# Kernel optimization log

Hardware: AMD Instinct MI355X
Metric: run time of the kernel (lower is better)

The kernel has to match this reference:

```python
import jax, jax.numpy as jnp
import numpy as np

IN_F = 8192
OUT_F = 8192
MAX_STATES = 100
THRESHOLD = MAX_STATES // 2  # 50
TARGET_FIRING_RATE = 0.1


def setup_inputs() -> dict:
    key = jax.random.key(0)
    k0, k1 = jax.random.split(key)
    spike_input = jax.random.uniform(k0, (IN_F,), dtype=jnp.float32)
    # buffer init: randint(threshold-5, threshold+5) -> values in [45, 55)
    synapse_states = jax.random.randint(k1, (OUT_F, IN_F), THRESHOLD - 5, THRESHOLD + 5).astype(jnp.float32)
    membrane_potential = jnp.zeros((OUT_F,), dtype=jnp.float32)
    adaptive_threshold = jnp.full((OUT_F,), 2.0, dtype=jnp.float32)
    eligibility_trace = jnp.zeros((OUT_F, IN_F), dtype=jnp.float32)
    return {
        "spike_input": spike_input,
        "synapse_states": synapse_states,
        "membrane_potential": membrane_potential,
        "adaptive_threshold": adaptive_threshold,
        "eligibility_trace": eligibility_trace,
    }


def reference(spike_input, synapse_states, membrane_potential, adaptive_threshold, eligibility_trace):
    # ternary (0/1) weights from state threshold
    w = (synapse_states > THRESHOLD).astype(jnp.float32)  # [out, in]
    x = jnp.clip(spike_input * 2.0, 0.0, 1.0)             # [in]
    current = jnp.einsum('oi,i->o', w, x)                 # [out]
    v_mem = membrane_potential * 0.7 + current            # decayed membrane + input current
    spikes = (v_mem >= adaptive_threshold).astype(jnp.float32)
    new_threshold = jnp.clip(adaptive_threshold + (spikes - TARGET_FIRING_RATE) * 0.05, 0.5, 5.0)
    new_trace = jnp.clip(eligibility_trace * 0.8 + jnp.outer(spikes, x), 0.0, 3.0)
    new_v_mem = v_mem * (1.0 - spikes) * 0.3              # reset fired neurons, leak rest
    return spikes, new_v_mem, new_threshold, new_trace
```

## Files before the change

kernel.cpp:

```cpp
#include <hip/hip_runtime.h>

#define IN_F 8192
#define OUT_F 8192
#define THRESHOLD_F 50.0f
#define TARGET_RATE 0.1f

__global__ __launch_bounds__(256, 4) void snn_fused_kernel(
    const float* __restrict__ spike_input,
    const float* __restrict__ synapse_states,
    const float* __restrict__ membrane_potential,
    const float* __restrict__ adaptive_threshold,
    const float* __restrict__ eligibility_trace,
    float* __restrict__ out_spikes,
    float* __restrict__ out_vmem,
    float* __restrict__ out_thresh,
    float* __restrict__ out_trace)
{
    __shared__ float xs[IN_F];
    __shared__ float wave_sum[4];
    __shared__ float s_spike;

    const int o   = blockIdx.x;
    const int tid = threadIdx.x;

    const float4* x4 = (const float4*)spike_input;
    float4* xs4 = (float4*)xs;
    #pragma unroll
    for (int k = 0; k < 8; ++k) {
        int idx = tid + k * 256;
        float4 v = x4[idx];
        v.x = fminf(fmaxf(v.x * 2.0f, 0.0f), 1.0f);
        v.y = fminf(fmaxf(v.y * 2.0f, 0.0f), 1.0f);
        v.z = fminf(fmaxf(v.z * 2.0f, 0.0f), 1.0f);
        v.w = fminf(fmaxf(v.w * 2.0f, 0.0f), 1.0f);
        xs4[idx] = v;
    }
    __syncthreads();

    const float4* s4 = (const float4*)(synapse_states + (size_t)o * IN_F);
    float sum = 0.0f;
    #pragma unroll
    for (int k = 0; k < 8; ++k) {
        int idx = tid + k * 256;
        float4 s = s4[idx];
        float4 v = xs4[idx];
        sum += (s.x > THRESHOLD_F ? v.x : 0.0f)
             + (s.y > THRESHOLD_F ? v.y : 0.0f)
             + (s.z > THRESHOLD_F ? v.z : 0.0f)
             + (s.w > THRESHOLD_F ? v.w : 0.0f);
    }
    #pragma unroll
    for (int off = 32; off > 0; off >>= 1)
        sum += __shfl_down(sum, off, 64);
    if ((tid & 63) == 0) wave_sum[tid >> 6] = sum;
    __syncthreads();

    if (tid == 0) {
        float current = wave_sum[0] + wave_sum[1] + wave_sum[2] + wave_sum[3];
        float v_mem = membrane_potential[o] * 0.7f + current;
        float thr   = adaptive_threshold[o];
        float spike = (v_mem >= thr) ? 1.0f : 0.0f;
        out_spikes[o] = spike;
        out_vmem[o]   = v_mem * (1.0f - spike) * 0.3f;
        out_thresh[o] = fminf(fmaxf(thr + (spike - TARGET_RATE) * 0.05f, 0.5f), 5.0f);
        s_spike = spike;
    }
    __syncthreads();
    const float spike = s_spike;

    const float4* e4 = (const float4*)(eligibility_trace + (size_t)o * IN_F);
    float4* t4 = (float4*)(out_trace + (size_t)o * IN_F);
    #pragma unroll
    for (int k = 0; k < 8; ++k) {
        int idx = tid + k * 256;
        float4 e = e4[idx];
        float4 v = xs4[idx];
        float4 t;
        t.x = fminf(fmaxf(e.x * 0.8f + spike * v.x, 0.0f), 3.0f);
        t.y = fminf(fmaxf(e.y * 0.8f + spike * v.y, 0.0f), 3.0f);
        t.z = fminf(fmaxf(e.z * 0.8f + spike * v.z, 0.0f), 3.0f);
        t.w = fminf(fmaxf(e.w * 0.8f + spike * v.w, 0.0f), 3.0f);
        t4[idx] = t;
    }
}

extern "C" void kernel_launch(void* const* d_in, const int* in_sizes, int n_in,
                              void* d_out, int out_size, void* d_ws, size_t ws_size,
                              hipStream_t stream) {
    const float* spike_input        = (const float*)d_in[0];
    const float* synapse_states     = (const float*)d_in[1];
    const float* membrane_potential = (const float*)d_in[2];
    const float* adaptive_threshold = (const float*)d_in[3];
    const float* eligibility_trace  = (const float*)d_in[4];

    float* out = (float*)d_out;
    float* out_spikes = out;
    float* out_vmem   = out + OUT_F;
    float* out_thresh = out + 2 * OUT_F;
    float* out_trace  = out + 3 * OUT_F;

    snn_fused_kernel<<<OUT_F, 256, 0, stream>>>(
        spike_input, synapse_states, membrane_potential, adaptive_threshold,
        eligibility_trace, out_spikes, out_vmem, out_thresh, out_trace);
}
```

Measured before the change: 587.4 us.

## Split fused SNN kernel into reduction and grid-stride trace update kernels

```diff
diff --git a/kernel.cpp b/kernel.cpp
--- a/kernel.cpp
+++ b/kernel.cpp
@@ -5,45 +5,33 @@
 #define THRESHOLD_F 50.0f
 #define TARGET_RATE 0.1f
 
-__global__ __launch_bounds__(256, 4) void snn_fused_kernel(
+__global__ __launch_bounds__(256) void snn_reduce_kernel(
     const float* __restrict__ spike_input,
     const float* __restrict__ synapse_states,
     const float* __restrict__ membrane_potential,
     const float* __restrict__ adaptive_threshold,
-    const float* __restrict__ eligibility_trace,
     float* __restrict__ out_spikes,
     float* __restrict__ out_vmem,
-    float* __restrict__ out_thresh,
-    float* __restrict__ out_trace)
+    float* __restrict__ out_thresh)
 {
-    __shared__ float xs[IN_F];
     __shared__ float wave_sum[4];
-    __shared__ float s_spike;
 
     const int o   = blockIdx.x;
     const int tid = threadIdx.x;
 
+    const float4* s4 = (const float4*)(synapse_states + (size_t)o * IN_F);
     const float4* x4 = (const float4*)spike_input;
-    float4* xs4 = (float4*)xs;
+
+    float sum = 0.0f;
     #pragma unroll
     for (int k = 0; k < 8; ++k) {
         int idx = tid + k * 256;
+        float4 s = s4[idx];
         float4 v = x4[idx];
         v.x = fminf(fmaxf(v.x * 2.0f, 0.0f), 1.0f);
         v.y = fminf(fmaxf(v.y * 2.0f, 0.0f), 1.0f);
         v.z = fminf(fmaxf(v.z * 2.0f, 0.0f), 1.0f);
         v.w = fminf(fmaxf(v.w * 2.0f, 0.0f), 1.0f);
-        xs4[idx] = v;
-    }
-    __syncthreads();
-
-    const float4* s4 = (const float4*)(synapse_states + (size_t)o * IN_F);
-    float sum = 0.0f;
-    #pragma unroll
-    for (int k = 0; k < 8; ++k) {
-        int idx = tid + k * 256;
-        float4 s = s4[idx];
-        float4 v = xs4[idx];
         sum += (s.x > THRESHOLD_F ? v.x : 0.0f)
              + (s.y > THRESHOLD_F ? v.y : 0.0f)
              + (s.z > THRESHOLD_F ? v.z : 0.0f)
@@ -63,23 +51,32 @@
         out_spikes[o] = spike;
         out_vmem[o]   = v_mem * (1.0f - spike) * 0.3f;
         out_thresh[o] = fminf(fmaxf(thr + (spike - TARGET_RATE) * 0.05f, 0.5f), 5.0f);
-        s_spike = spike;
     }
-    __syncthreads();
-    const float spike = s_spike;
+}
 
-    const float4* e4 = (const float4*)(eligibility_trace + (size_t)o * IN_F);
-    float4* t4 = (float4*)(out_trace + (size_t)o * IN_F);
-    #pragma unroll
-    for (int k = 0; k < 8; ++k) {
-        int idx = tid + k * 256;
+__global__ __launch_bounds__(256) void snn_trace_kernel(
+    const float* __restrict__ spike_input,
+    const float* __restrict__ eligibility_trace,
+    const float* __restrict__ out_spikes,
+    float* __restrict__ out_trace)
+{
+    const int total4 = (OUT_F * IN_F) / 4;
+    const int nthreads = gridDim.x * blockDim.x;
+    const float4* e4 = (const float4*)eligibility_trace;
+    const float4* x4 = (const float4*)spike_input;
+    float4* t4 = (float4*)out_trace;
+
+    for (int idx = blockIdx.x * blockDim.x + threadIdx.x; idx < total4; idx += nthreads) {
+        int row = idx >> 11;
+        int col = idx & 2047;
+        float  spike = out_spikes[row];
         float4 e = e4[idx];
-        float4 v = xs4[idx];
+        float4 v = x4[col];
         float4 t;
-        t.x = fminf(fmaxf(e.x * 0.8f + spike * v.x, 0.0f), 3.0f);
-        t.y = fminf(fmaxf(e.y * 0.8f + spike * v.y, 0.0f), 3.0f);
-        t.z = fminf(fmaxf(e.z * 0.8f + spike * v.z, 0.0f), 3.0f);
-        t.w = fminf(fmaxf(e.w * 0.8f + spike * v.w, 0.0f), 3.0f);
+        t.x = fminf(fmaxf(e.x * 0.8f + spike * fminf(fmaxf(v.x * 2.0f, 0.0f), 1.0f), 0.0f), 3.0f);
+        t.y = fminf(fmaxf(e.y * 0.8f + spike * fminf(fmaxf(v.y * 2.0f, 0.0f), 1.0f), 0.0f), 3.0f);
+        t.z = fminf(fmaxf(e.z * 0.8f + spike * fminf(fmaxf(v.z * 2.0f, 0.0f), 1.0f), 0.0f), 3.0f);
+        t.w = fminf(fmaxf(e.w * 0.8f + spike * fminf(fmaxf(v.w * 2.0f, 0.0f), 1.0f), 0.0f), 3.0f);
         t4[idx] = t;
     }
 }
@@ -99,7 +96,10 @@
     float* out_thresh = out + 2 * OUT_F;
     float* out_trace  = out + 3 * OUT_F;
 
-    snn_fused_kernel<<<OUT_F, 256, 0, stream>>>(
+    snn_reduce_kernel<<<OUT_F, 256, 0, stream>>>(
         spike_input, synapse_states, membrane_potential, adaptive_threshold,
-        eligibility_trace, out_spikes, out_vmem, out_thresh, out_trace);
+        out_spikes, out_vmem, out_thresh);
+
+    snn_trace_kernel<<<8192, 256, 0, stream>>>(
+        spike_input, eligibility_trace, out_spikes, out_trace);
 }
```

Measured after the change: 582.3 us. Within noise of the previous version (-0.9%).
